# Performance work log

Hardware: AMD Instinct MI355X
Metric: run time of the kernel (lower is better)

The kernel has to match this reference:

```python
import jax, jax.numpy as jnp
import numpy as np

NUM_ROI = 200

def mish(x):
    return x * jnp.tanh(jax.nn.softplus(x))

def gcn_conv(x, edge_index, edge_weight, W, b):
    # PyG GCNConv: add self-loops (weight 1), symmetric normalization, aggregate at target (col)
    N = x.shape[0]
    row, col = edge_index[0], edge_index[1]
    loop = jnp.arange(N)
    row = jnp.concatenate([row, loop])
    col = jnp.concatenate([col, loop])
    w = jnp.concatenate([edge_weight, jnp.ones((N,), x.dtype)])
    deg = jax.ops.segment_sum(w, col, num_segments=N)
    dis = jnp.where(deg > 0, jax.lax.rsqrt(deg), 0.0)
    norm = dis[row] * w * dis[col]                       # [E+N]
    h = x @ W                                            # [N, out]
    out = jax.ops.segment_sum(h[row] * norm[:, None], col, num_segments=N)
    return out + b

def setup_inputs() -> dict:
    key = jax.random.key(0)
    ks = jax.random.split(key, 16)
    B, E = 256, 1638400
    N = B * NUM_ROI
    d = {}
    d['x'] = jax.random.normal(ks[0], (N, NUM_ROI), jnp.float32)
    d['edge_index'] = jax.random.randint(ks[1], (2, E), 0, N, jnp.int64)
    d['edge_attr'] = jax.random.uniform(ks[2], (E,), jnp.float32)
    def rn(k, shape, fan_in):
        return jax.random.normal(k, shape, jnp.float32) * (1.0 / np.sqrt(fan_in))
    d['W1'] = rn(ks[3], (NUM_ROI, 128), NUM_ROI); d['b1'] = jnp.zeros((128,), jnp.float32)
    d['W2'] = rn(ks[4], (128, 64), 128);          d['b2'] = jnp.zeros((64,), jnp.float32)
    d['Wro'] = rn(ks[5], (64, 8), 64);            d['bro'] = jnp.zeros((8,), jnp.float32)
    d['Wfc1'] = rn(ks[6], (8 * NUM_ROI, NUM_ROI), 8 * NUM_ROI); d['bfc1'] = jnp.zeros((NUM_ROI,), jnp.float32)
    d['bn_gamma'] = jnp.ones((NUM_ROI,), jnp.float32)
    d['bn_beta'] = jnp.zeros((NUM_ROI,), jnp.float32)
    d['Wfc2'] = rn(ks[7], (NUM_ROI, 2), NUM_ROI); d['bfc2'] = jnp.zeros((2,), jnp.float32)
    d['Wd1'] = rn(ks[8], (NUM_ROI, 64), NUM_ROI); d['bd1'] = jnp.zeros((64,), jnp.float32)
    d['Wd2'] = rn(ks[9], (64, 6), 64);            d['bd2'] = jnp.zeros((6,), jnp.float32)
    return d

def reference(x, edge_index, edge_attr, W1, b1, W2, b2, Wro, bro, Wfc1, bfc1,
              bn_gamma, bn_beta, Wfc2, bfc2, Wd1, bd1, Wd2, bd2):
    h = mish(gcn_conv(x, edge_index, edge_attr, W1, b1))
    h = mish(gcn_conv(h, edge_index, edge_attr, W2, b2))
    out = mish(h @ Wro + bro)                            # [N, 8]
    feat = out.reshape(-1, NUM_ROI * 8)                  # [B, 1600]
    z = feat @ Wfc1 + bfc1                               # [B, numROI]
    # BatchNorm1d in training mode (batch statistics, biased variance)
    mu = jnp.mean(z, axis=0)
    var = jnp.mean((z - mu) ** 2, axis=0)
    zn = (z - mu) * jax.lax.rsqrt(var + 1e-5) * bn_gamma + bn_beta
    mid = mish(zn)
    logits = mid @ Wfc2 + bfc2                           # [B, 2]
    rev = 2.0 * jax.lax.stop_gradient(mid) - mid
    cls_logits = jax.nn.relu(rev @ Wd1 + bd1) @ Wd2 + bd2  # [B, 6]
    return (logits, cls_logits)
```

## Files before the change

### kernel.cpp

```cpp
#include <hip/hip_runtime.h>
#include <hip/hip_bf16.h>

typedef __hip_bfloat16 bf16;
typedef __attribute__((ext_vector_type(8))) short short8;
typedef __attribute__((ext_vector_type(4))) float f32x4;

#define NROI 200
#define EPB 12800
#define SPB 6400

__device__ __forceinline__ float u2f(unsigned short u) {
  return __uint_as_float(((unsigned)u) << 16);
}
__device__ __forceinline__ float lo16(unsigned u) { return __uint_as_float(u << 16); }
__device__ __forceinline__ float hi16(unsigned u) { return __uint_as_float(u & 0xffff0000u); }
__device__ __forceinline__ float b2f(bf16 v) { return __bfloat162float(v); }
__device__ __forceinline__ unsigned short f2us(float f) {
  union { bf16 b; unsigned short u; } c;
  c.b = __float2bfloat16(f);
  return c.u;
}

__device__ __forceinline__ float mishf(float x) {
  float sp = (x > 20.0f) ? x : log1pf(expf(x));
  return x * tanhf(sp);
}

__global__ __launch_bounds__(256) void detect_kernel(const unsigned short* xu,
                                                     const unsigned* eiw,
                                                     int* flags) {
  int tid = threadIdx.x;
  int sane = 0, zodd = 0;
  for (int i = tid; i < 4096; i += 256) {
    unsigned short u = xu[2 * i];
    unsigned e = (u >> 7) & 0xFF;
    if (u == 0 || (e >= 100 && e <= 134)) sane++;
  }
  for (int i = tid; i < 4096; i += 256) {
    if (eiw[2 * i + 1] == 0) zodd++;
  }
  __shared__ int s1[256], s2[256];
  s1[tid] = sane; s2[tid] = zodd;
  __syncthreads();
  for (int off = 128; off > 0; off >>= 1) {
    if (tid < off) { s1[tid] += s1[tid + off]; s2[tid] += s2[tid + off]; }
    __syncthreads();
  }
  if (tid == 0) {
    flags[0] = (s1[0] < 2048) ? 1 : 0;
    flags[1] = (s2[0] > 2048) ? 1 : 0;
  }
}

struct WArgs {
  const void* src[16];
  int n[16];
  int off[16];
};

__global__ __launch_bounds__(256) void convert_weights(WArgs a, bf16* base,
                                                       const int* flags) {
  int t = blockIdx.y;
  int i = blockIdx.x * 256 + threadIdx.x;
  if (i >= a.n[t]) return;
  bf16* dst = base + a.off[t];
  if (flags[0]) dst[i] = __float2bfloat16(((const float*)a.src[t])[i]);
  else ((unsigned short*)dst)[i] = ((const unsigned short*)a.src[t])[i];
}

__device__ __forceinline__ void swz_one(const unsigned short* src,
                                        unsigned short* dst, int idx,
                                        int K, int NT) {
  int e = idx & 7;
  int l = (idx >> 3) & 63;
  int t = (idx >> 9) % NT;
  int kc = idx / (NT * 512);
  int k = kc * 32 + (l >> 4) * 8 + e;
  int c = t * 16 + (l & 15);
  dst[idx] = (k < K) ? src[k * (NT * 16) + c] : 0;
}

__global__ __launch_bounds__(256) void prep_kernel(const unsigned short* __restrict__ w1,
                                                   const unsigned short* __restrict__ w2,
                                                   unsigned short* __restrict__ w1swz,
                                                   unsigned short* __restrict__ w2swz,
                                                   int b1, int b2) {
  int i = blockIdx.x * 256 + threadIdx.x;
  if (i < b1) swz_one(w1, w1swz, i, 200, 8);
  else if (i < b2) swz_one(w2, w2swz, i - b1, 128, 4);
}


__global__ __launch_bounds__(1024, 1) void count_lds(const int* __restrict__ ei,
                                                     const void* __restrict__ ea,
                                                     const int* __restrict__ flags,
                                                     unsigned* __restrict__ cnt8g,
                                                     unsigned* __restrict__ ws16g,
                                                     unsigned char* __restrict__ rank8,
                                                     int NU, int NW, int E) {
  extern __shared__ unsigned smem[];
  unsigned* s_cnt = smem;
  unsigned* s_ws  = smem + NU;
  int tid = threadIdx.x;
  int blk = blockIdx.x;
  for (int i = tid; i < NU + NW; i += 1024) smem[i] = 0;
  __syncthreads();
  int is64 = flags[1], isf32 = flags[0];
  long long base = (long long)blk * EPB;
  for (int k = 0; k < EPB; k += 1024) {
    int ko = k + tid;
    long long e = base + ko;
    if (ko < EPB && e < E) {
      int c = is64 ? __builtin_nontemporal_load(&ei[2 * ((long long)E + e)])
                   : __builtin_nontemporal_load(&ei[(long long)E + e]);
      float w = isf32 ? __builtin_nontemporal_load(&((const float*)ea)[e])
                      : u2f(__builtin_nontemporal_load(&((const unsigned short*)ea)[e]));
      w = fminf(fmaxf(w, 0.0f), 15.0f);
      unsigned sh = (unsigned)(c & 3) * 8;
      unsigned old = atomicAdd(&s_cnt[c >> 2], 1u << sh);
      rank8[e] = (unsigned char)((old >> sh) & 0xFF);
      unsigned wi = __float2uint_rn(w * 4096.0f);
      atomicAdd(&s_ws[c >> 1], (c & 1) ? (wi << 16) : wi);
    }
  }
  __syncthreads();
  for (int i = tid; i < NU; i += 1024)
    __builtin_nontemporal_store(s_cnt[i], &cnt8g[(size_t)blk * NU + i]);
  for (int i = tid; i < NW; i += 1024)
    __builtin_nontemporal_store(s_ws[i], &ws16g[(size_t)blk * NW + i]);
}

__global__ __launch_bounds__(256) void reduce_r1(unsigned* __restrict__ cnt8g,
                                                 const unsigned* __restrict__ ws16g,
                                                 unsigned* __restrict__ cntpart,
                                                 unsigned* __restrict__ wspart,
                                                 int NU, int NW, int nblk, int bpg) {
  int col = blockIdx.x * 256 + threadIdx.x;
  int gy = blockIdx.y;
  if (col >= NU) return;
  unsigned run = 0;
  unsigned r0 = 0, r1 = 0, r2 = 0, r3 = 0;
  int b0 = gy * bpg;
  int be = b0 + bpg; if (be > nblk) be = nblk;
  for (int b = b0; b < be; ++b) {
    unsigned v = cnt8g[(size_t)b * NU + col];
    cnt8g[(size_t)b * NU + col] = run;
    run += v;
    unsigned wA = ws16g[(size_t)b * NW + 2 * col];
    unsigned wB = ws16g[(size_t)b * NW + 2 * col + 1];
    r0 += wA & 0xFFFF; r1 += wA >> 16;
    r2 += wB & 0xFFFF; r3 += wB >> 16;
  }
  cntpart[(size_t)gy * NU + col] = run;
  unsigned* wp = &wspart[((size_t)gy * NU + col) * 4];
  wp[0] = r0; wp[1] = r1; wp[2] = r2; wp[3] = r3;
}

__global__ __launch_bounds__(256) void combine_k(const unsigned* __restrict__ cntpart,
                                                 const unsigned* __restrict__ wspart,
                                                 unsigned* __restrict__ gybase,
                                                 int* __restrict__ cnt,
                                                 float* __restrict__ dis,
                                                 int* __restrict__ bsum,
                                                 int NU, int N) {
  __shared__ int ts[256];
  int col = blockIdx.x * 256 + threadIdx.x;
  int mysum = 0;
  if (col < NU) {
    unsigned g = 0;
#pragma unroll
    for (int gy = 0; gy < 4; ++gy) {
      unsigned t = cntpart[(size_t)gy * NU + col];
      gybase[(size_t)gy * NU + col] = g;
      g += t;
    }
    unsigned ws[4] = {0, 0, 0, 0};
#pragma unroll
    for (int gy = 0; gy < 4; ++gy) {
      const unsigned* wp = &wspart[((size_t)gy * NU + col) * 4];
#pragma unroll
      for (int j = 0; j < 4; ++j) ws[j] += wp[j];
    }
#pragma unroll
    for (int j = 0; j < 4; ++j) {
      int n = 4 * col + j;
      if (n < N) {
        int cj = (int)((g >> (8 * j)) & 0xFF);
        cnt[n] = cj;
        mysum += cj;
        dis[n] = rsqrtf(1.0f + (float)ws[j] * 0.000244140625f);
      }
    }
  }
  int tid = threadIdx.x;
  ts[tid] = mysum;
  __syncthreads();
  for (int off = 128; off > 0; off >>= 1) {
    if (tid < off) ts[tid] += ts[tid + off];
    __syncthreads();
  }
  if (tid == 0) bsum[blockIdx.x] = ts[0];
}

__global__ __launch_bounds__(64) void scan_phase2(const int* __restrict__ bsum,
                                                  int* __restrict__ bpre,
                                                  int* __restrict__ ptr, int nb, int N) {
  if (threadIdx.x == 0) {
    int run = 0;
    for (int i = 0; i < nb; ++i) { bpre[i] = run; run += bsum[i]; }
    ptr[N] = run;
  }
}

__global__ __launch_bounds__(256) void scan_phase3(const int* __restrict__ cnt,
                                                   const int* __restrict__ bpre,
                                                   int* __restrict__ ptr, int N) {
  __shared__ int ts[256];
  int tid = threadIdx.x;
  int base = blockIdx.x * 1024 + tid * 4;
  int c0 = 0, c1 = 0, c2 = 0, c3 = 0;
  if (base + 0 < N) c0 = cnt[base + 0];
  if (base + 1 < N) c1 = cnt[base + 1];
  if (base + 2 < N) c2 = cnt[base + 2];
  if (base + 3 < N) c3 = cnt[base + 3];
  ts[tid] = c0 + c1 + c2 + c3;
  __syncthreads();
  for (int off = 1; off < 256; off <<= 1) {
    int v = ts[tid];
    if (tid >= off) v += ts[tid - off];
    __syncthreads();
    ts[tid] = v;
    __syncthreads();
  }
  int run = bpre[blockIdx.x] + (tid ? ts[tid - 1] : 0);
  if (base + 0 < N) { ptr[base + 0] = run; run += c0; }
  if (base + 1 < N) { ptr[base + 1] = run; run += c1; }
  if (base + 2 < N) { ptr[base + 2] = run; run += c2; }
  if (base + 3 < N) { ptr[base + 3] = run; run += c3; }
}

__global__ __launch_bounds__(1024, 1) void scatter_lds(const int* __restrict__ ei,
                                                       const void* __restrict__ ea,
                                                       const int* __restrict__ flags,
                                                       const float* __restrict__ dis,
                                                       const int* __restrict__ ptr,
                                                       const unsigned* __restrict__ cnt8g,
                                                       const unsigned* __restrict__ gybase,
                                                       const unsigned char* __restrict__ rank8,
                                                       long long* __restrict__ epair,
                                                       int NU, int bpg, int E) {
  extern __shared__ unsigned smem[];
  unsigned* s_pb = smem;
  unsigned* s_gb = smem + NU;
  int tid = threadIdx.x;
  int blk = blockIdx.x;
  int cblk = blk >> 1;
  int gy = cblk / bpg;
  for (int i = tid; i < NU; i += 1024) s_pb[i] = cnt8g[(size_t)cblk * NU + i];
  for (int i = tid; i < NU; i += 1024) s_gb[i] = gybase[(size_t)gy * NU + i];
  __syncthreads();
  int is64 = flags[1], isf32 = flags[0];
  long long base = (long long)blk * SPB;
  for (int k = 0; k < SPB; k += 1024) {
    int ko = k + tid;
    long long e = base + ko;
    if (ko < SPB && e < E) {
      int r = is64 ? __builtin_nontemporal_load(&ei[2 * e])
                   : __builtin_nontemporal_load(&ei[e]);
      int c = is64 ? __builtin_nontemporal_load(&ei[2 * ((long long)E + e)])
                   : __builtin_nontemporal_load(&ei[(long long)E + e]);
      float w = isf32 ? __builtin_nontemporal_load(&((const float*)ea)[e])
                      : u2f(__builtin_nontemporal_load(&((const unsigned short*)ea)[e]));
      float nrm = dis[r] * w * dis[c];
      unsigned sh = (unsigned)(c & 3) * 8;
      unsigned p1 = (s_pb[c >> 2] >> sh) & 0xFF;
      unsigned p2 = (s_gb[c >> 2] >> sh) & 0xFF;
      int idx = ptr[c] + (int)p1 + (int)p2 + (int)rank8[e];
      long long pr = (long long)((unsigned long long)__float_as_uint(nrm) << 32) |
                     (unsigned)r;
      __builtin_nontemporal_store(pr, &epair[idx]);
    }
  }
}

template<int KC, int NT, int DYN>
__global__ __launch_bounds__(256) void gemm_mfma(const void* __restrict__ A,
                                                 int Ktrue,
                                                 const int* __restrict__ flags,
                                                 const unsigned short* __restrict__ Wswz,
                                                 unsigned short* __restrict__ H,
                                                 int M) {
  int wid = threadIdx.x >> 6, lane = threadIdx.x & 63;
  int row0 = (blockIdx.x * 4 + wid) * 16;
  if (row0 >= M) return;
  constexpr int NC = NT * 16;
  int isf32 = DYN ? flags[0] : 0;
  f32x4 acc[NT];
#pragma unroll
  for (int t = 0; t < NT; ++t) acc[t] = {0.f, 0.f, 0.f, 0.f};
  int arow = row0 + (lane & 15);
  int kbase = (lane >> 4) * 8;
  const float* Af = (const float*)A;
  const unsigned short* Au = (const unsigned short*)A;
#pragma unroll
  for (int kc = 0; kc < KC; ++kc) {
    int k0 = kbase + kc * 32;
    short8 a = {0, 0, 0, 0, 0, 0, 0, 0};
    if (k0 + 8 <= Ktrue) {
      size_t off = (size_t)arow * Ktrue + k0;
      if (DYN && isf32) {
        f32x4 f0 = __builtin_nontemporal_load((const f32x4*)&Af[off]);
        f32x4 f1 = __builtin_nontemporal_load((const f32x4*)&Af[off + 4]);
        a[0] = (short)f2us(f0[0]); a[1] = (short)f2us(f0[1]);
        a[2] = (short)f2us(f0[2]); a[3] = (short)f2us(f0[3]);
        a[4] = (short)f2us(f1[0]); a[5] = (short)f2us(f1[1]);
        a[6] = (short)f2us(f1[2]); a[7] = (short)f2us(f1[3]);
      } else {
        a = *(const short8*)&Au[off];
      }
    }
#pragma unroll
    for (int t = 0; t < NT; ++t) {
      short8 b = *(const short8*)&Wswz[((kc * NT + t) * 64 + lane) * 8];
      acc[t] = __builtin_amdgcn_mfma_f32_16x16x32_bf16(a, b, acc[t], 0, 0, 0);
    }
  }
  int orow = row0 + (lane >> 4) * 4;
  int ocol = lane & 15;
#pragma unroll
  for (int t = 0; t < NT; ++t)
#pragma unroll
    for (int r = 0; r < 4; ++r)
      H[(size_t)(orow + r) * NC + t * 16 + ocol] = f2us(acc[t][r]);
}

__global__ __launch_bounds__(256) void agg_mish128(const unsigned* __restrict__ hu,
                                                   const float* __restrict__ dis,
                                                   const int* __restrict__ ptr,
                                                   const long long* __restrict__ ep,
                                                   const bf16* __restrict__ bias,
                                                   unsigned* __restrict__ g, int N) {
  int w = threadIdx.x >> 6, lane = threadIdx.x & 63;
  int n = blockIdx.x * 4 + w;
  float dn = dis[n];
  float self = dn * dn;
  unsigned u = hu[((unsigned)n << 6) + lane];
  float acc0 = lo16(u) * self;
  float acc1 = hi16(u) * self;
  int e0 = ptr[n], e1 = ptr[n + 1];
  for (int base = e0; base < e1; base += 64) {
    long long myp = 0;
    if (base + lane < e1) myp = __builtin_nontemporal_load(&ep[base + lane]);
    int mx = (int)(unsigned)myp;
    int my = (int)(myp >> 32);
    int m = e1 - base; if (m > 64) m = 64;
    int j = 0;
    for (; j + 8 <= m; j += 8) {
      unsigned uu[8]; float ww[8];
#pragma unroll
      for (int q = 0; q < 8; ++q) {
        unsigned rr = (unsigned)__builtin_amdgcn_readlane(mx, j + q);
        uu[q] = hu[(rr << 6) + lane];
        ww[q] = __uint_as_float(__builtin_amdgcn_readlane(my, j + q));
      }
#pragma unroll
      for (int q = 0; q < 8; ++q) {
        acc0 += lo16(uu[q]) * ww[q];
        acc1 += hi16(uu[q]) * ww[q];
      }
    }
    for (; j < m; ++j) {
      unsigned rr = (unsigned)__builtin_amdgcn_readlane(mx, j);
      float ww = __uint_as_float(__builtin_amdgcn_readlane(my, j));
      unsigned uu = hu[(rr << 6) + lane];
      acc0 += lo16(uu) * ww;
      acc1 += hi16(uu) * ww;
    }
  }
  unsigned bb = ((const unsigned*)bias)[lane];
  float m0 = mishf(acc0 + lo16(bb));
  float m1 = mishf(acc1 + hi16(bb));
  __builtin_nontemporal_store(((unsigned)f2us(m1) << 16) | f2us(m0),
                              &g[((unsigned)n << 6) + lane]);
}

__global__ __launch_bounds__(256) void agg_mish64_ro(const unsigned short* __restrict__ hus,
                                                     const float* __restrict__ dis,
                                                     const int* __restrict__ ptr,
                                                     const long long* __restrict__ ep,
                                                     const bf16* __restrict__ bias,
                                                     const bf16* __restrict__ Wro,
                                                     const bf16* __restrict__ bro,
                                                     float* __restrict__ out8, int N) {
  int w = threadIdx.x >> 6, lane = threadIdx.x & 63;
  int n = blockIdx.x * 4 + w;
  float dn = dis[n];
  float self = dn * dn;
  float acc = u2f(hus[((unsigned)n << 6) + lane]) * self;
  int e0 = ptr[n], e1 = ptr[n + 1];
  for (int base = e0; base < e1; base += 64) {
    long long myp = 0;
    if (base + lane < e1) myp = __builtin_nontemporal_load(&ep[base + lane]);
    int mx = (int)(unsigned)myp;
    int my = (int)(myp >> 32);
    int m = e1 - base; if (m > 64) m = 64;
    int j = 0;
    for (; j + 8 <= m; j += 8) {
      float vv[8], ww[8];
#pragma unroll
      for (int q = 0; q < 8; ++q) {
        unsigned rr = (unsigned)__builtin_amdgcn_readlane(mx, j + q);
        vv[q] = u2f(hus[(rr << 6) + lane]);
        ww[q] = __uint_as_float(__builtin_amdgcn_readlane(my, j + q));
      }
#pragma unroll
      for (int q = 0; q < 8; ++q) acc += vv[q] * ww[q];
    }
    for (; j < m; ++j) {
      unsigned rr = (unsigned)__builtin_amdgcn_readlane(mx, j);
      float ww = __uint_as_float(__builtin_amdgcn_readlane(my, j));
      acc += u2f(hus[(rr << 6) + lane]) * ww;
    }
  }
  float mv = mishf(acc + u2f(((const unsigned short*)bias)[lane]));
  uint4 wr = ((const uint4*)Wro)[lane];
  float p0 = mv * lo16(wr.x), p1 = mv * hi16(wr.x);
  float p2 = mv * lo16(wr.y), p3 = mv * hi16(wr.y);
  float p4 = mv * lo16(wr.z), p5 = mv * hi16(wr.z);
  float p6 = mv * lo16(wr.w), p7 = mv * hi16(wr.w);
  bool b0 = lane & 1;
  float q0 = (b0 ? p4 : p0) + __shfl_xor(b0 ? p0 : p4, 1);
  float q1 = (b0 ? p5 : p1) + __shfl_xor(b0 ? p1 : p5, 1);
  float q2 = (b0 ? p6 : p2) + __shfl_xor(b0 ? p2 : p6, 1);
  float q3 = (b0 ? p7 : p3) + __shfl_xor(b0 ? p3 : p7, 1);
  bool b1 = lane & 2;
  float r0 = (b1 ? q2 : q0) + __shfl_xor(b1 ? q0 : q2, 2);
  float r1 = (b1 ? q3 : q1) + __shfl_xor(b1 ? q1 : q3, 2);
  bool b2v = lane & 4;
  float t = (b2v ? r1 : r0) + __shfl_xor(b2v ? r0 : r1, 4);
  t += __shfl_xor(t, 8);
  t += __shfl_xor(t, 16);
  t += __shfl_xor(t, 32);
  if (lane < 8) {
    int oidx = ((lane & 1) << 2) | (lane & 2) | ((lane >> 2) & 1);
    out8[(size_t)n * 8 + oidx] = mishf(t + u2f(((const unsigned short*)bro)[oidx]));
  }
}


__global__ __launch_bounds__(256) void fc1_kernel(const float* __restrict__ feat,
                                                  const bf16* __restrict__ W,
                                                  const bf16* __restrict__ bias,
                                                  float* __restrict__ z) {
  __shared__ float fr[1600];
  int b = blockIdx.x, tid = threadIdx.x;
  for (int i = tid; i < 1600; i += 256) fr[i] = feat[(size_t)b * 1600 + i];
  __syncthreads();
  if (tid < NROI) {
    float acc = b2f(bias[tid]);
#pragma unroll 8
    for (int k = 0; k < 1600; ++k) acc += fr[k] * b2f(W[k * NROI + tid]);
    z[b * NROI + tid] = acc;
  }
}

__global__ __launch_bounds__(256) void bn_stats(const float* __restrict__ z,
                                                float* mu, float* rvar, int B) {
  int j = blockIdx.x;
  int tid = threadIdx.x;
  float v = z[tid * NROI + j];
  float s = v, q = v * v;
  for (int off = 32; off > 0; off >>= 1) {
    s += __shfl_down(s, off);
    q += __shfl_down(q, off);
  }
  __shared__ float ss[4], qq[4];
  int w = tid >> 6, lane = tid & 63;
  if (lane == 0) { ss[w] = s; qq[w] = q; }
  __syncthreads();
  if (tid == 0) {
    float S = ss[0] + ss[1] + ss[2] + ss[3];
    float Q = qq[0] + qq[1] + qq[2] + qq[3];
    float m = S / (float)B;
    float var = Q / (float)B - m * m;
    mu[j] = m;
    rvar[j] = rsqrtf(var + 1e-5f);
  }
}

__global__ __launch_bounds__(256) void head_kernel(const float* __restrict__ z,
                                                   const float* __restrict__ mu,
                                                   const float* __restrict__ rvar,
                                                   const bf16* __restrict__ gamma,
                                                   const bf16* __restrict__ beta,
                                                   const bf16* __restrict__ Wfc2,
                                                   const bf16* __restrict__ bfc2,
                                                   const bf16* __restrict__ Wd1,
                                                   const bf16* __restrict__ bd1,
                                                   const bf16* __restrict__ Wd2,
                                                   const bf16* __restrict__ bd2,
                                                   float* __restrict__ out, int B) {
  __shared__ float mid[NROI];
  __shared__ float t[64];
  int b = blockIdx.x, tid = threadIdx.x;
  if (tid < NROI) {
    float v = (z[b * NROI + tid] - mu[tid]) * rvar[tid] * b2f(gamma[tid]) + b2f(beta[tid]);
    mid[tid] = mishf(v);
  }
  __syncthreads();
  if (tid < 64) {
    float acc = b2f(bd1[tid]);
#pragma unroll 8
    for (int j = 0; j < NROI; ++j) acc += mid[j] * b2f(Wd1[j * 64 + tid]);
    t[tid] = fmaxf(acc, 0.0f);
  }
  if (tid >= 64 && tid < 66) {
    int c = tid - 64;
    float acc = b2f(bfc2[c]);
    for (int j = 0; j < NROI; ++j) acc += mid[j] * b2f(Wfc2[j * 2 + c]);
    out[b * 2 + c] = acc;
  }
  __syncthreads();
  if (tid < 6) {
    float acc = b2f(bd2[tid]);
#pragma unroll 8
    for (int k = 0; k < 64; ++k) acc += t[k] * b2f(Wd2[k * 6 + tid]);
    out[B * 2 + b * 6 + tid] = acc;
  }
}


extern "C" void kernel_launch(void* const* d_in, const int* in_sizes, int n_in,
                              void* d_out, int out_size, void* d_ws, size_t ws_size,
                              hipStream_t stream) {
  const void* x  = d_in[0];
  const int*  ei = (const int*)d_in[1];
  const void* ea = d_in[2];
  float* out = (float*)d_out;

  int N = in_sizes[0] / NROI;
  int E = in_sizes[2];
  int B = N / NROI;

  int NU = (N + 3) / 4;
  int NW = (N + 1) / 2;
  int nblk = (E + EPB - 1) / EPB;
  int bpg = (nblk + 3) / 4;
  int nsb = (E + SPB - 1) / SPB;

  char* p = (char*)d_ws;
  auto carve = [&](size_t bytes) -> void* {
    void* r = (void*)p;
    p += (bytes + 255) & ~(size_t)255;
    return r;
  };
  int*   flags = (int*)carve(16);
  bf16*  cw    = (bf16*)carve(400000 * 2);
  float* dis   = (float*)carve((size_t)N * 4);
  unsigned* cnt8g  = (unsigned*)carve((size_t)nblk * NU * 4);
  unsigned* ws16g  = (unsigned*)carve((size_t)nblk * NW * 4);
  unsigned* cntpart = (unsigned*)carve((size_t)4 * NU * 4);
  unsigned* wspart  = (unsigned*)carve((size_t)4 * NU * 16);
  unsigned* gybase  = (unsigned*)carve((size_t)4 * NU * 4);
  unsigned char* rank8 = (unsigned char*)carve((size_t)E);
  int*   cnt   = (int*)carve((size_t)N * 4);
  int*   ptr   = (int*)carve(((size_t)N + 1) * 4);
  int*   bsum  = (int*)carve(1024);
  int*   bpre  = (int*)carve(1024);
  long long* epair = (long long*)carve((size_t)E * 8);
  unsigned short* h = (unsigned short*)carve((size_t)N * 128 * 2);
  unsigned* g = (unsigned*)carve((size_t)N * 128 * 2);
  unsigned short* w1swz = (unsigned short*)carve(7 * 8 * 512 * 2);
  unsigned short* w2swz = (unsigned short*)carve(4 * 4 * 512 * 2);
  float* out8  = (float*)carve((size_t)N * 8 * 4);
  float* z     = (float*)carve((size_t)B * NROI * 4);
  float* mu    = (float*)carve(NROI * 4);
  float* rv    = (float*)carve(NROI * 4);

  WArgs wa;
  int run = 0;
  int maxn = 0;
  for (int t = 0; t < 16; ++t) {
    wa.src[t] = d_in[3 + t];
    wa.n[t]   = in_sizes[3 + t];
    wa.off[t] = run;
    run += in_sizes[3 + t];
    if (in_sizes[3 + t] > maxn) maxn = in_sizes[3 + t];
  }
  const bf16* W1   = cw + wa.off[0];
  const bf16* b1   = cw + wa.off[1];
  const bf16* W2   = cw + wa.off[2];
  const bf16* b2   = cw + wa.off[3];
  const bf16* Wro  = cw + wa.off[4];
  const bf16* bro  = cw + wa.off[5];
  const bf16* Wfc1 = cw + wa.off[6];
  const bf16* bfc1 = cw + wa.off[7];
  const bf16* gam  = cw + wa.off[8];
  const bf16* bet  = cw + wa.off[9];
  const bf16* Wfc2 = cw + wa.off[10];
  const bf16* bfc2 = cw + wa.off[11];
  const bf16* Wd1  = cw + wa.off[12];
  const bf16* bd1  = cw + wa.off[13];
  const bf16* Wd2  = cw + wa.off[14];
  const bf16* bd2  = cw + wa.off[15];

  detect_kernel<<<1, 256, 0, stream>>>((const unsigned short*)x,
                                       (const unsigned*)ei, flags);
  dim3 wg((maxn + 255) / 256, 16);
  convert_weights<<<wg, 256, 0, stream>>>(wa, cw, flags);

  int pb1 = 7 * 8 * 512;
  int pb2 = pb1 + 4 * 4 * 512;
  prep_kernel<<<(pb2 + 255) / 256, 256, 0, stream>>>(
      (const unsigned short*)W1, (const unsigned short*)W2, w1swz, w2swz,
      pb1, pb2);

  size_t cntLds = (size_t)(NU + NW) * 4;
  count_lds<<<nblk, 1024, cntLds, stream>>>(ei, ea, flags, cnt8g, ws16g,
                                            rank8, NU, NW, E);
  dim3 rg((NU + 255) / 256, 4);
  reduce_r1<<<rg, 256, 0, stream>>>(cnt8g, ws16g, cntpart, wspart,
                                    NU, NW, nblk, bpg);
  int ncomb = (NU + 255) / 256;
  combine_k<<<ncomb, 256, 0, stream>>>(cntpart, wspart, gybase, cnt, dis,
                                       bsum, NU, N);
  scan_phase2<<<1, 64, 0, stream>>>(bsum, bpre, ptr, ncomb, N);
  scan_phase3<<<ncomb, 256, 0, stream>>>(cnt, bpre, ptr, N);

  size_t scLds = (size_t)2 * NU * 4;
  scatter_lds<<<nsb, 1024, scLds, stream>>>(ei, ea, flags, dis, ptr, cnt8g,
                                            gybase, rank8, epair, NU, bpg, E);

  gemm_mfma<7, 8, 1><<<N / 64, 256, 0, stream>>>(x, 200, flags, w1swz, h, N);
  agg_mish128<<<N / 4, 256, 0, stream>>>((const unsigned*)h, dis, ptr, epair,
                                         b1, g, N);
  gemm_mfma<4, 4, 0><<<N / 64, 256, 0, stream>>>(g, 128, flags, w2swz, h, N);
  agg_mish64_ro<<<N / 4, 256, 0, stream>>>(h, dis, ptr, epair, b2, Wro, bro,
                                           out8, N);

  fc1_kernel<<<B, 256, 0, stream>>>(out8, Wfc1, bfc1, z);
  bn_stats<<<NROI, 256, 0, stream>>>(z, mu, rv, B);
  head_kernel<<<B, 256, 0, stream>>>(z, mu, rv, gam, bet, Wfc2, bfc2,
                                     Wd1, bd1, Wd2, bd2, out, B);
}
```

Before: 364.6 us.

## Fuse prep kernels, drop scan phase2, halve count block size

```diff
diff --git a/kernel.cpp b/kernel.cpp
--- a/kernel.cpp
+++ b/kernel.cpp
@@ -6,7 +6,7 @@
 typedef __attribute__((ext_vector_type(4))) float f32x4;
 
 #define NROI 200
-#define EPB 12800
+#define EPB 6400
 #define SPB 6400
 
 __device__ __forceinline__ float u2f(unsigned short u) {
@@ -59,35 +59,38 @@
 };
 
 __global__ __launch_bounds__(256) void convert_weights(WArgs a, bf16* base,
+                                                       unsigned short* __restrict__ w1swz,
+                                                       unsigned short* __restrict__ w2swz,
                                                        const int* flags) {
   int t = blockIdx.y;
   int i = blockIdx.x * 256 + threadIdx.x;
-  if (i >= a.n[t]) return;
-  bf16* dst = base + a.off[t];
-  if (flags[0]) dst[i] = __float2bfloat16(((const float*)a.src[t])[i]);
-  else ((unsigned short*)dst)[i] = ((const unsigned short*)a.src[t])[i];
-}
-
-__device__ __forceinline__ void swz_one(const unsigned short* src,
-                                        unsigned short* dst, int idx,
-                                        int K, int NT) {
-  int e = idx & 7;
-  int l = (idx >> 3) & 63;
-  int t = (idx >> 9) % NT;
-  int kc = idx / (NT * 512);
+  int isf32 = flags[0];
+  if (t < 16) {
+    if (i >= a.n[t]) return;
+    bf16* dst = base + a.off[t];
+    if (isf32) dst[i] = __float2bfloat16(((const float*)a.src[t])[i]);
+    else ((unsigned short*)dst)[i] = ((const unsigned short*)a.src[t])[i];
+    return;
+  }
+  int w1 = (t == 16);
+  int K  = w1 ? 200 : 128;
+  int NT = w1 ? 8 : 4;
+  int KC = w1 ? 7 : 4;
+  int total = KC * NT * 512;
+  if (i >= total) return;
+  int e = i & 7;
+  int l = (i >> 3) & 63;
+  int tt = (i >> 9) % NT;
+  int kc = i / (NT * 512);
   int k = kc * 32 + (l >> 4) * 8 + e;
-  int c = t * 16 + (l & 15);
-  dst[idx] = (k < K) ? src[k * (NT * 16) + c] : 0;
-}
-
-__global__ __launch_bounds__(256) void prep_kernel(const unsigned short* __restrict__ w1,
-                                                   const unsigned short* __restrict__ w2,
-                                                   unsigned short* __restrict__ w1swz,
-                                                   unsigned short* __restrict__ w2swz,
-                                                   int b1, int b2) {
-  int i = blockIdx.x * 256 + threadIdx.x;
-  if (i < b1) swz_one(w1, w1swz, i, 200, 8);
-  else if (i < b2) swz_one(w2, w2swz, i - b1, 128, 4);
+  int c = tt * 16 + (l & 15);
+  unsigned short v = 0;
+  if (k < K) {
+    const void* src = w1 ? a.src[0] : a.src[2];
+    if (isf32) v = f2us(((const float*)src)[k * (NT * 16) + c]);
+    else v = ((const unsigned short*)src)[k * (NT * 16) + c];
+  }
+  (w1 ? w1swz : w2swz)[i] = v;
 }
 
 
@@ -202,22 +205,16 @@
   if (tid == 0) bsum[blockIdx.x] = ts[0];
 }
 
-__global__ __launch_bounds__(64) void scan_phase2(const int* __restrict__ bsum,
-                                                  int* __restrict__ bpre,
-                                                  int* __restrict__ ptr, int nb, int N) {
-  if (threadIdx.x == 0) {
-    int run = 0;
-    for (int i = 0; i < nb; ++i) { bpre[i] = run; run += bsum[i]; }
-    ptr[N] = run;
-  }
-}
-
 __global__ __launch_bounds__(256) void scan_phase3(const int* __restrict__ cnt,
-                                                   const int* __restrict__ bpre,
-                                                   int* __restrict__ ptr, int N) {
+                                                   const int* __restrict__ bsum,
+                                                   int* __restrict__ ptr,
+                                                   int nb, int N) {
   __shared__ int ts[256];
+  int blk = blockIdx.x;
   int tid = threadIdx.x;
-  int base = blockIdx.x * 1024 + tid * 4;
+  int bpre = 0;
+  for (int i = 0; i < blk; ++i) bpre += bsum[i];
+  int base = blk * 1024 + tid * 4;
   int c0 = 0, c1 = 0, c2 = 0, c3 = 0;
   if (base + 0 < N) c0 = cnt[base + 0];
   if (base + 1 < N) c1 = cnt[base + 1];
@@ -232,11 +229,12 @@
     ts[tid] = v;
     __syncthreads();
   }
-  int run = bpre[blockIdx.x] + (tid ? ts[tid - 1] : 0);
+  int run = bpre + (tid ? ts[tid - 1] : 0);
   if (base + 0 < N) { ptr[base + 0] = run; run += c0; }
   if (base + 1 < N) { ptr[base + 1] = run; run += c1; }
   if (base + 2 < N) { ptr[base + 2] = run; run += c2; }
   if (base + 3 < N) { ptr[base + 3] = run; run += c3; }
+  if (blk == nb - 1 && tid == 255) ptr[N] = bpre + ts[255];
 }
 
 __global__ __launch_bounds__(1024, 1) void scatter_lds(const int* __restrict__ ei,
@@ -254,9 +252,8 @@
   unsigned* s_gb = smem + NU;
   int tid = threadIdx.x;
   int blk = blockIdx.x;
-  int cblk = blk >> 1;
-  int gy = cblk / bpg;
-  for (int i = tid; i < NU; i += 1024) s_pb[i] = cnt8g[(size_t)cblk * NU + i];
+  int gy = blk / bpg;
+  for (int i = tid; i < NU; i += 1024) s_pb[i] = cnt8g[(size_t)blk * NU + i];
   for (int i = tid; i < NU; i += 1024) s_gb[i] = gybase[(size_t)gy * NU + i];
   __syncthreads();
   int is64 = flags[1], isf32 = flags[0];
@@ -566,7 +563,6 @@
   int*   cnt   = (int*)carve((size_t)N * 4);
   int*   ptr   = (int*)carve(((size_t)N + 1) * 4);
   int*   bsum  = (int*)carve(1024);
-  int*   bpre  = (int*)carve(1024);
   long long* epair = (long long*)carve((size_t)E * 8);
   unsigned short* h = (unsigned short*)carve((size_t)N * 128 * 2);
   unsigned* g = (unsigned*)carve((size_t)N * 128 * 2);
@@ -606,14 +602,8 @@
 
   detect_kernel<<<1, 256, 0, stream>>>((const unsigned short*)x,
                                        (const unsigned*)ei, flags);
-  dim3 wg((maxn + 255) / 256, 16);
-  convert_weights<<<wg, 256, 0, stream>>>(wa, cw, flags);
-
-  int pb1 = 7 * 8 * 512;
-  int pb2 = pb1 + 4 * 4 * 512;
-  prep_kernel<<<(pb2 + 255) / 256, 256, 0, stream>>>(
-      (const unsigned short*)W1, (const unsigned short*)W2, w1swz, w2swz,
-      pb1, pb2);
+  dim3 wg((maxn + 255) / 256, 18);
+  convert_weights<<<wg, 256, 0, stream>>>(wa, cw, w1swz, w2swz, flags);
 
   size_t cntLds = (size_t)(NU + NW) * 4;
   count_lds<<<nblk, 1024, cntLds, stream>>>(ei, ea, flags, cnt8g, ws16g,
@@ -624,8 +614,7 @@
   int ncomb = (NU + 255) / 256;
   combine_k<<<ncomb, 256, 0, stream>>>(cntpart, wspart, gybase, cnt, dis,
                                        bsum, NU, N);
-  scan_phase2<<<1, 64, 0, stream>>>(bsum, bpre, ptr, ncomb, N);
-  scan_phase3<<<ncomb, 256, 0, stream>>>(cnt, bpre, ptr, N);
+  scan_phase3<<<ncomb, 256, 0, stream>>>(cnt, bsum, ptr, ncomb, N);
 
   size_t scLds = (size_t)2 * NU * 4;
   scatter_lds<<<nsb, 1024, scLds, stream>>>(ei, ea, flags, dis, ptr, cnt8g,
```

Result: slower. 376.0 us (+3.1%).
